# Performance work log

Measured on AMD Instinct MI355X. Metric: run time of the kernel, lower is better.

## Reference

```python
import jax, jax.numpy as jnp
import numpy as np

N = 100000
E = 1600000
F_IN = 128
HID = 64
HEADS = 2
OUT_HEADS = 1
NUM_CLASS = 18
NEG_SLOPE = 0.2


def setup_inputs() -> dict:
    key = jax.random.key(0)
    ks = jax.random.split(key, 12)
    x = jax.random.normal(ks[0], (N, F_IN), dtype=jnp.float32)
    edge_index = jax.random.randint(ks[1], (2, E), 0, N, dtype=jnp.int64)
    s = lambda k, shp, fan: jax.random.normal(k, shp, dtype=jnp.float32) * (1.0 / np.sqrt(fan))
    W0 = s(ks[2], (F_IN, HID), F_IN)
    b0 = jnp.zeros((HID,), dtype=jnp.float32)
    W1 = s(ks[3], (HID, HEADS * HID), HID)
    att_src1 = s(ks[4], (HEADS, HID), HID)
    att_dst1 = s(ks[5], (HEADS, HID), HID)
    b1 = jnp.zeros((HEADS * HID,), dtype=jnp.float32)
    W2 = s(ks[6], (HEADS * HID, OUT_HEADS * NUM_CLASS), HEADS * HID)
    att_src2 = s(ks[7], (OUT_HEADS, NUM_CLASS), NUM_CLASS)
    att_dst2 = s(ks[8], (OUT_HEADS, NUM_CLASS), NUM_CLASS)
    b2 = jnp.zeros((OUT_HEADS * NUM_CLASS,), dtype=jnp.float32)
    return {"x": x, "edge_index": edge_index, "W0": W0, "b0": b0,
            "W1": W1, "att_src1": att_src1, "att_dst1": att_dst1, "b1": b1,
            "W2": W2, "att_src2": att_src2, "att_dst2": att_dst2, "b2": b2}


def gat_conv(x, src, dst, W, att_s, att_d, bias, heads, out_ch):
    n = x.shape[0]
    h = (x @ W).reshape(n, heads, out_ch)              # [N,H,C]
    a_s = jnp.sum(h * att_s, axis=-1)                   # [N,H]
    a_d = jnp.sum(h * att_d, axis=-1)                   # [N,H]
    e = jax.nn.leaky_relu(a_s[src] + a_d[dst], NEG_SLOPE)  # [E,H]
    m = jax.ops.segment_max(e, dst, num_segments=n)
    ex = jnp.exp(e - m[dst])
    denom = jax.ops.segment_sum(ex, dst, num_segments=n)
    alpha = ex / denom[dst]                              # [E,H]
    msg = h[src] * alpha[:, :, None]                     # [E,H,C]
    out = jax.ops.segment_sum(msg, dst, num_segments=n)  # [N,H,C]
    return out.reshape(n, heads * out_ch) + bias


def reference(x, edge_index, W0, b0, W1, att_src1, att_dst1, b1, W2, att_src2, att_dst2, b2):
    n = x.shape[0]
    # PyG GATConv adds self-loops by default
    loops = jnp.arange(n, dtype=edge_index.dtype)
    src = jnp.concatenate([edge_index[0], loops])
    dst = jnp.concatenate([edge_index[1], loops])
    # eval mode: dropout is identity
    h = jax.nn.relu(x @ W0 + b0)
    h = jax.nn.elu(gat_conv(h, src, dst, W1, att_src1, att_dst1, b1, HEADS, HID))
    out = gat_conv(h, src, dst, W2, att_src2, att_dst2, b2, OUT_HEADS, NUM_CLASS)
    return jax.nn.log_softmax(out, axis=-1)
```

## Files before the change

kernel.cpp:

```cpp
#include <hip/hip_runtime.h>
#include <math.h>


#define NEG_SLOPE 0.2f
#define STASH_CAP 128

typedef unsigned short ushort_t;

__device__ __forceinline__ float wmax(float v) {
    for (int o = 32; o; o >>= 1) v = fmaxf(v, __shfl_xor(v, o));
    return v;
}
__device__ __forceinline__ float wsum(float v) {
    for (int o = 32; o; o >>= 1) v += __shfl_xor(v, o);
    return v;
}

__device__ __forceinline__ unsigned bfpack(float a, float b) {
    unsigned ua = __float_as_uint(a);
    unsigned ub = __float_as_uint(b);
    ua = (ua + 0x7fffu + ((ua >> 16) & 1u)) >> 16;
    ub = (ub + 0x7fffu + ((ub >> 16) & 1u)) & 0xffff0000u;
    return ua | ub;
}
__device__ __forceinline__ ushort_t bf16of(float a) {
    unsigned ua = __float_as_uint(a);
    return (ushort_t)((ua + 0x7fffu + ((ua >> 16) & 1u)) >> 16);
}
__device__ __forceinline__ float bflo(unsigned u) { return __uint_as_float(u << 16); }
__device__ __forceinline__ float bfhi(unsigned u) { return __uint_as_float(u & 0xffff0000u); }
__device__ __forceinline__ float bfval(ushort_t u) { return __uint_as_float(((unsigned)u) << 16); }

__global__ void k_deg_init(int* __restrict__ deg, int N) {
    int i = blockIdx.x * blockDim.x + threadIdx.x;
    if (i < N) deg[i] = 1;
}

__global__ __launch_bounds__(256) void k_deg_edges(const int* __restrict__ ei,
                                                   int* __restrict__ deg,
                                                   int E, int cohortBlocks) {
    int c = blockIdx.x & 7;
    int pb = blockIdx.x >> 3;
    int tid = pb * 256 + threadIdx.x;
    int stride = cohortBlocks * 256;
    for (int e = tid; e < E; e += stride) {
        int dst = ei[E + e];
        if (((dst >> 13) & 7) != c) continue;
        atomicAdd(&deg[dst], 1);
    }
}

__global__ __launch_bounds__(256) void k_scan1(const int* __restrict__ deg, int* __restrict__ rs,
                                               int* __restrict__ bsum, int N) {
    __shared__ int s[256];
    int t = threadIdx.x;
    int base = blockIdx.x * 1024;
    int i0 = base + t * 4;
    int d0 = (i0 + 0 < N) ? deg[i0 + 0] : 0;
    int d1 = (i0 + 1 < N) ? deg[i0 + 1] : 0;
    int d2 = (i0 + 2 < N) ? deg[i0 + 2] : 0;
    int d3 = (i0 + 3 < N) ? deg[i0 + 3] : 0;
    int s0 = d0, s1 = s0 + d1, s2 = s1 + d2, s3 = s2 + d3;
    int tsum = s3;
    s[t] = tsum;
    __syncthreads();
    for (int off = 1; off < 256; off <<= 1) {
        int v = (t >= off) ? s[t - off] : 0;
        __syncthreads();
        s[t] += v;
        __syncthreads();
    }
    int excl = s[t] - tsum;
    if (i0 + 0 < N) rs[1 + i0 + 0] = excl + s0;
    if (i0 + 1 < N) rs[1 + i0 + 1] = excl + s1;
    if (i0 + 2 < N) rs[1 + i0 + 2] = excl + s2;
    if (i0 + 3 < N) rs[1 + i0 + 3] = excl + s3;
    if (t == 0) bsum[blockIdx.x] = s[255];
}

__global__ __launch_bounds__(256) void k_scan2(const int* __restrict__ bsum,
                                               int* __restrict__ boff, int NB) {
    __shared__ int s[256];
    int t = threadIdx.x;
    int orig = (t < NB) ? bsum[t] : 0;
    s[t] = orig;
    __syncthreads();
    for (int off = 1; off < 256; off <<= 1) {
        int v = (t >= off) ? s[t - off] : 0;
        __syncthreads();
        s[t] += v;
        __syncthreads();
    }
    if (t < NB) boff[t] = s[t] - orig;
}

__global__ void k_scan3(int* __restrict__ rs, const int* __restrict__ boff,
                        const int* __restrict__ deg, int* __restrict__ cursor, int N) {
    int i = blockIdx.x * blockDim.x + threadIdx.x;
    if (i == 0) rs[0] = 0;
    if (i < N) {
        int v = rs[1 + i] + boff[i >> 10];
        rs[1 + i] = v;
        cursor[i] = v - deg[i] + 1;
    }
}

__global__ __launch_bounds__(256) void k_scatter(const int* __restrict__ ei,
                                                 int* __restrict__ cursor,
                                                 const int* __restrict__ rs,
                                                 int* __restrict__ csr,
                                                 int E, int Etot, int cohortBlocks) {
    int c = blockIdx.x & 7;
    int pb = blockIdx.x >> 3;
    int tid = pb * 256 + threadIdx.x;
    int stride = cohortBlocks * 256;
    for (int e = tid; e < Etot; e += stride) {
        int dst = (e < E) ? ei[E + e] : (e - E);
        if (((dst >> 13) & 7) != c) continue;
        if (e < E) {
            int pos = atomicAdd(&cursor[dst], 1);
            csr[pos] = ei[e];
        } else {
            csr[rs[dst]] = dst;
        }
    }
}

__global__ __launch_bounds__(256) void k_gemm12(const float* __restrict__ x,
                                                const float* __restrict__ W0,
                                                const float* __restrict__ b0,
                                                const float* __restrict__ W1,
                                                const float* __restrict__ as_g,
                                                const float* __restrict__ ad_g,
                                                ushort_t* __restrict__ h1b,
                                                float* __restrict__ as1,
                                                float* __restrict__ ad1, int N) {
    __shared__ float smem[16640];
    float* al  = smem;
    float* wl  = smem + 8448;
    float* al2 = smem;
    int t = threadIdx.x;
    int n0 = blockIdx.x * 64;
    {
        const float4* wg = (const float4*)W0;
        float4* wl4 = (float4*)wl;
#pragma unroll
        for (int i = 0; i < 8; ++i) wl4[t + i * 256] = wg[t + i * 256];
#pragma unroll
        for (int i = 0; i < 8; ++i) {
            int f = t + i * 256;
            int node = f >> 5, q = f & 31;
            int ng = n0 + node; if (ng > N - 1) ng = N - 1;
            float4 v = ((const float4*)x)[(size_t)ng * 32 + q];
            *(float4*)&al[node * 132 + q * 4] = v;
        }
    }
    __syncthreads();
    int colg = t & 15;
    int rowg = t >> 4;
    float4 acc[4];
#pragma unroll
    for (int j = 0; j < 4; ++j) acc[j] = make_float4(0.f, 0.f, 0.f, 0.f);
    for (int k4 = 0; k4 < 128; k4 += 4) {
        float4 w0 = *(float4*)&wl[(k4 + 0) * 64 + colg * 4];
        float4 w1 = *(float4*)&wl[(k4 + 1) * 64 + colg * 4];
        float4 w2 = *(float4*)&wl[(k4 + 2) * 64 + colg * 4];
        float4 w3 = *(float4*)&wl[(k4 + 3) * 64 + colg * 4];
#pragma unroll
        for (int j = 0; j < 4; ++j) {
            float4 a = *(float4*)&al[(rowg * 4 + j) * 132 + k4];
            acc[j].x += a.x * w0.x + a.y * w1.x + a.z * w2.x + a.w * w3.x;
            acc[j].y += a.x * w0.y + a.y * w1.y + a.z * w2.y + a.w * w3.y;
            acc[j].z += a.x * w0.z + a.y * w1.z + a.z * w2.z + a.w * w3.z;
            acc[j].w += a.x * w0.w + a.y * w1.w + a.z * w2.w + a.w * w3.w;
        }
    }
    float4 bb = ((const float4*)b0)[colg];
    float4 h0v[4];
#pragma unroll
    for (int j = 0; j < 4; ++j) {
        h0v[j].x = fmaxf(acc[j].x + bb.x, 0.f);
        h0v[j].y = fmaxf(acc[j].y + bb.y, 0.f);
        h0v[j].z = fmaxf(acc[j].z + bb.z, 0.f);
        h0v[j].w = fmaxf(acc[j].w + bb.w, 0.f);
    }
    __syncthreads();
#pragma unroll
    for (int j = 0; j < 4; ++j)
        *(float4*)&al2[(rowg * 4 + j) * 68 + colg * 4] = h0v[j];
    {
        const float4* wg1 = (const float4*)W1;
        float4* wl4 = (float4*)wl;
#pragma unroll
        for (int i = 0; i < 8; ++i) wl4[t + i * 256] = wg1[t + i * 256];
    }
    __syncthreads();
    int colg2 = t & 31;
    int rowg2 = t >> 5;
    float4 acc2[8];
#pragma unroll
    for (int j = 0; j < 8; ++j) acc2[j] = make_float4(0.f, 0.f, 0.f, 0.f);
    for (int k4 = 0; k4 < 64; k4 += 4) {
        float4 w0 = *(float4*)&wl[(k4 + 0) * 128 + colg2 * 4];
        float4 w1 = *(float4*)&wl[(k4 + 1) * 128 + colg2 * 4];
        float4 w2 = *(float4*)&wl[(k4 + 2) * 128 + colg2 * 4];
        float4 w3 = *(float4*)&wl[(k4 + 3) * 128 + colg2 * 4];
#pragma unroll
        for (int j = 0; j < 8; ++j) {
            float4 a = *(float4*)&al2[(rowg2 * 8 + j) * 68 + k4];
            acc2[j].x += a.x * w0.x + a.y * w1.x + a.z * w2.x + a.w * w3.x;
            acc2[j].y += a.x * w0.y + a.y * w1.y + a.z * w2.y + a.w * w3.y;
            acc2[j].z += a.x * w0.z + a.y * w1.z + a.z * w2.z + a.w * w3.z;
            acc2[j].w += a.x * w0.w + a.y * w1.w + a.z * w2.w + a.w * w3.w;
        }
    }
    float4 asv = ((const float4*)as_g)[colg2];
    float4 adv = ((const float4*)ad_g)[colg2];
    float ps[8], pd[8];
#pragma unroll
    for (int j = 0; j < 8; ++j) {
        ps[j] = acc2[j].x * asv.x + acc2[j].y * asv.y + acc2[j].z * asv.z + acc2[j].w * asv.w;
        pd[j] = acc2[j].x * adv.x + acc2[j].y * adv.y + acc2[j].z * adv.z + acc2[j].w * adv.w;
    }
    for (int o = 1; o < 16; o <<= 1) {
#pragma unroll
        for (int j = 0; j < 8; ++j) {
            ps[j] += __shfl_xor(ps[j], o);
            pd[j] += __shfl_xor(pd[j], o);
        }
    }
#pragma unroll
    for (int j = 0; j < 8; ++j) {
        int n = n0 + rowg2 * 8 + j;
        if (n < N) {
            uint2 pr;
            pr.x = bfpack(acc2[j].x, acc2[j].y);
            pr.y = bfpack(acc2[j].z, acc2[j].w);
            ((uint2*)h1b)[(size_t)n * 32 + colg2] = pr;
        }
    }
    int lane = t & 63;
    if ((lane & 15) == 0) {
        int head = (lane >> 4) & 1;
#pragma unroll
        for (int j = 0; j < 8; ++j) {
            int n = n0 + rowg2 * 8 + j;
            if (n < N) {
                as1[n * 2 + head] = ps[j];
                ad1[n * 2 + head] = pd[j];
            }
        }
    }
}

__global__ __launch_bounds__(256) void k_node_l1(const int* __restrict__ rs,
                                                 const int* __restrict__ csr,
                                                 const ushort_t* __restrict__ h1b,
                                                 const float* __restrict__ as1,
                                                 const float* __restrict__ ad1,
                                                 const float* __restrict__ b1,
                                                 unsigned* __restrict__ aggb, int N) {
    __shared__ float2 stashA[4][128];
    __shared__ float4 stashE[4][STASH_CAP];
    int wid = threadIdx.x >> 6;
    int lane = threadIdx.x & 63;
    int n = (blockIdx.x * 256 + threadIdx.x) >> 6;
    if (n >= N) return;
    int row = rs[n], end = rs[n + 1];
    int deg = end - row;
    float2 adv = ((const float2*)ad1)[n];
    const float2* asp = (const float2*)as1;
    const char* h1base = (const char*)h1b;
    int eg = lane >> 4;
    int fl = lane & 15;
    int head_off = (fl >= 8) ? 64 : 0;
    int flbase = fl * 16;
    float acc[8] = {0.f, 0.f, 0.f, 0.f, 0.f, 0.f, 0.f, 0.f};
    float inv0, inv1;
    if (deg <= 64) {
        bool act = lane < deg;
        int src = act ? csr[row + lane] : 0;
        float2 av = asp[src];
        float e0 = av.x + adv.x, e1 = av.y + adv.y;
        e0 = e0 > 0.f ? e0 : NEG_SLOPE * e0;
        e1 = e1 > 0.f ? e1 : NEG_SLOPE * e1;
        if (!act) { e0 = -INFINITY; e1 = -INFINITY; }
        float m0 = wmax(e0), m1 = wmax(e1);
        float p0 = act ? __expf(e0 - m0) : 0.f;
        float p1 = act ? __expf(e1 - m1) : 0.f;
        inv0 = __builtin_amdgcn_rcpf(wsum(p0));
        inv1 = __builtin_amdgcn_rcpf(wsum(p1));
        stashA[wid][lane] = make_float2(__int_as_float(src), p0);
        stashA[wid][64 + lane] = make_float2(__int_as_float(src), p1);
        int deg8 = (deg + 7) & ~7;
        int b0i = head_off + eg;
        float2 sa0 = stashA[wid][b0i];
        float2 sa1 = stashA[wid][b0i + 4];
        uint4 u0 = *(const uint4*)(h1base + (((unsigned)__float_as_int(sa0.x)) << 8) + flbase);
        uint4 u1 = *(const uint4*)(h1base + (((unsigned)__float_as_int(sa1.x)) << 8) + flbase);
        for (int j = 0; j < deg8; j += 8) {
            int jn = (j + 8 < deg8) ? j + 8 : 0;
            float2 sb0 = stashA[wid][b0i + jn];
            float2 sb1 = stashA[wid][b0i + jn + 4];
            uint4 v0 = *(const uint4*)(h1base + (((unsigned)__float_as_int(sb0.x)) << 8) + flbase);
            uint4 v1 = *(const uint4*)(h1base + (((unsigned)__float_as_int(sb1.x)) << 8) + flbase);
            float a0 = sa0.y, a1 = sa1.y;
            acc[0] += bflo(u0.x) * a0; acc[1] += bfhi(u0.x) * a0;
            acc[2] += bflo(u0.y) * a0; acc[3] += bfhi(u0.y) * a0;
            acc[4] += bflo(u0.z) * a0; acc[5] += bfhi(u0.z) * a0;
            acc[6] += bflo(u0.w) * a0; acc[7] += bfhi(u0.w) * a0;
            acc[0] += bflo(u1.x) * a1; acc[1] += bfhi(u1.x) * a1;
            acc[2] += bflo(u1.y) * a1; acc[3] += bfhi(u1.y) * a1;
            acc[4] += bflo(u1.z) * a1; acc[5] += bfhi(u1.z) * a1;
            acc[6] += bflo(u1.w) * a1; acc[7] += bfhi(u1.w) * a1;
            sa0 = sb0; sa1 = sb1; u0 = v0; u1 = v1;
        }
    } else {
        inv0 = 1.f; inv1 = 1.f;
        float m0 = -INFINITY, m1 = -INFINITY, l0 = 0.f, l1 = 0.f;
        for (int base = row; base < end; base += 64) {
            int idx = base + lane;
            bool act = idx < end;
            int src = act ? csr[idx] : 0;
            float2 av = asp[src];
            float e0 = av.x + adv.x, e1 = av.y + adv.y;
            e0 = e0 > 0.f ? e0 : NEG_SLOPE * e0;
            e1 = e1 > 0.f ? e1 : NEG_SLOPE * e1;
            int sidx = idx - row;
            if (act && sidx < STASH_CAP)
                stashE[wid][sidx] = make_float4(__int_as_float(src), e0, e1, 0.f);
            if (!act) { e0 = -INFINITY; e1 = -INFINITY; }
            float m0n = fmaxf(m0, wmax(e0));
            float m1n = fmaxf(m1, wmax(e1));
            float p0 = act ? __expf(e0 - m0n) : 0.f;
            float p1 = act ? __expf(e1 - m1n) : 0.f;
            l0 = l0 * __expf(m0 - m0n) + wsum(p0);
            l1 = l1 * __expf(m1 - m1n) + wsum(p1);
            m0 = m0n; m1 = m1n;
        }
        float r0 = __builtin_amdgcn_rcpf(l0);
        float r1 = __builtin_amdgcn_rcpf(l1);
        for (int base = row; base < end; base += 64) {
            int idx = base + lane;
            bool act = idx < end;
            int sidx = idx - row;
            int src; float e0, e1;
            if (sidx < STASH_CAP) {
                float4 se = stashE[wid][sidx];
                src = __float_as_int(se.x);
                e0 = se.y; e1 = se.z;
            } else {
                src = act ? csr[idx] : 0;
                float2 av = asp[src];
                e0 = av.x + adv.x; e1 = av.y + adv.y;
                e0 = e0 > 0.f ? e0 : NEG_SLOPE * e0;
                e1 = e1 > 0.f ? e1 : NEG_SLOPE * e1;
            }
            if (!act) src = 0;
            float a0 = act ? __expf(e0 - m0) * r0 : 0.f;
            float a1 = act ? __expf(e1 - m1) * r1 : 0.f;
            stashA[wid][lane] = make_float2(__int_as_float(src), a0);
            stashA[wid][64 + lane] = make_float2(__int_as_float(src), a1);
            int cnt = min(64, end - base);
            for (int j = 0; j < cnt; j += 4) {
                float2 sa = stashA[wid][head_off + j + eg];
                int sj = __float_as_int(sa.x);
                float aj = sa.y;
                uint4 u = *(const uint4*)(h1base + (((unsigned)sj) << 8) + flbase);
                acc[0] += bflo(u.x) * aj; acc[1] += bfhi(u.x) * aj;
                acc[2] += bflo(u.y) * aj; acc[3] += bfhi(u.y) * aj;
                acc[4] += bflo(u.z) * aj; acc[5] += bfhi(u.z) * aj;
                acc[6] += bflo(u.w) * aj; acc[7] += bfhi(u.w) * aj;
            }
        }
    }
#pragma unroll
    for (int i = 0; i < 8; ++i) {
        acc[i] += __shfl_xor(acc[i], 16);
        acc[i] += __shfl_xor(acc[i], 32);
    }
    if (lane < 16) {
        float inv = (lane >= 8) ? inv1 : inv0;
        float4 ba = ((const float4*)b1)[lane * 2];
        float4 bb4 = ((const float4*)b1)[lane * 2 + 1];
        float v[8];
        v[0] = acc[0] * inv + ba.x;  v[1] = acc[1] * inv + ba.y;
        v[2] = acc[2] * inv + ba.z;  v[3] = acc[3] * inv + ba.w;
        v[4] = acc[4] * inv + bb4.x; v[5] = acc[5] * inv + bb4.y;
        v[6] = acc[6] * inv + bb4.z; v[7] = acc[7] * inv + bb4.w;
#pragma unroll
        for (int i = 0; i < 8; ++i) v[i] = v[i] > 0.f ? v[i] : __expf(v[i]) - 1.f;
        uint4 pk;
        pk.x = bfpack(v[0], v[1]); pk.y = bfpack(v[2], v[3]);
        pk.z = bfpack(v[4], v[5]); pk.w = bfpack(v[6], v[7]);
        ((uint4*)aggb)[(size_t)n * 16 + lane] = pk;
    }
}

__global__ __launch_bounds__(256, 4) void k_node2(const unsigned* __restrict__ aggb,
                                                  const float* __restrict__ W2,
                                                  const float* __restrict__ as_g,
                                                  const float* __restrict__ ad_g,
                                                  ushort_t* __restrict__ h2b,
                                                  float* __restrict__ a_s,
                                                  float* __restrict__ a_d, int N) {
    __shared__ float al[64 * 132];
    __shared__ float w2t[20 * 132];
    int t = threadIdx.x;
    int n0 = blockIdx.x * 64;
#pragma unroll
    for (int i = 0; i < 4; ++i) {
        int f = t + i * 256;
        int node = f >> 4, q = f & 15;
        int ng = n0 + node; if (ng > N - 1) ng = N - 1;
        uint4 u = ((const uint4*)aggb)[(size_t)ng * 16 + q];
        float* dst = &al[node * 132 + q * 8];
        dst[0] = bflo(u.x); dst[1] = bfhi(u.x);
        dst[2] = bflo(u.y); dst[3] = bfhi(u.y);
        dst[4] = bflo(u.z); dst[5] = bfhi(u.z);
        dst[6] = bflo(u.w); dst[7] = bfhi(u.w);
    }
    for (int i = t; i < 2560; i += 256) {
        int c = i >> 7, k = i & 127;
        w2t[c * 132 + k] = (c < 18) ? W2[k * 18 + c] : 0.f;
    }
    __syncthreads();
    int node = t >> 2;
    int cq = t & 3;
    int c0 = cq * 5;
    int n = n0 + node;
    float acc[5] = {0.f, 0.f, 0.f, 0.f, 0.f};
#pragma unroll 2
    for (int k4 = 0; k4 < 128; k4 += 4) {
        float4 a = *(float4*)&al[node * 132 + k4];
#pragma unroll
        for (int i = 0; i < 5; ++i) {
            float4 w = *(float4*)&w2t[(c0 + i) * 132 + k4];
            acc[i] += a.x * w.x + a.y * w.y + a.z * w.z + a.w * w.w;
        }
    }
    float ps = 0.f, pd = 0.f;
#pragma unroll
    for (int i = 0; i < 5; ++i) {
        int c = c0 + i;
        float asv = (c < 18) ? as_g[c] : 0.f;
        float adv = (c < 18) ? ad_g[c] : 0.f;
        ps += acc[i] * asv;
        pd += acc[i] * adv;
    }
    ps += __shfl_xor(ps, 1); ps += __shfl_xor(ps, 2);
    pd += __shfl_xor(pd, 1); pd += __shfl_xor(pd, 2);
    if (n < N) {
#pragma unroll
        for (int i = 0; i < 5; ++i) {
            int c = c0 + i;
            if (c < 18) h2b[(size_t)n * 32 + c] = bf16of(acc[i]);
        }
        if (cq == 0) { a_s[n] = ps; a_d[n] = pd; }
    }
}

__global__ __launch_bounds__(256) void k_node_l2(const int* __restrict__ rs,
                                                 const int* __restrict__ csr,
                                                 const ushort_t* __restrict__ h2b,
                                                 const float* __restrict__ as2,
                                                 const float* __restrict__ ad2,
                                                 const float* __restrict__ b2,
                                                 float* __restrict__ out, int N) {
    __shared__ float2 stash[4][STASH_CAP];
    int wid = threadIdx.x >> 6;
    int lane = threadIdx.x & 63;
    int n = (blockIdx.x * 256 + threadIdx.x) >> 6;
    if (n >= N) return;
    int row = rs[n], end = rs[n + 1];
    int deg = end - row;
    float adn = ad2[n];
    int g = lane / 21;
    int c = lane - g * 21;
    int cc = c < 18 ? c : 17;
    float acc = 0.f;
    float post;
    if (deg <= 64) {
        bool act = lane < deg;
        int src = act ? csr[row + lane] : 0;
        float e = as2[src] + adn;
        e = e > 0.f ? e : NEG_SLOPE * e;
        if (!act) e = -INFINITY;
        float m = wmax(e);
        float p = act ? __expf(e - m) : 0.f;
        post = __builtin_amdgcn_rcpf(wsum(p));
        stash[wid][lane] = make_float2(__int_as_float(src), p);
        int o = g;
        for (; o + 3 < deg; o += 6) {
            float2 s0 = stash[wid][o];
            float2 s1 = stash[wid][o + 3];
            int q0 = __float_as_int(s0.x);
            int q1 = __float_as_int(s1.x);
            float v0 = bfval(h2b[(size_t)q0 * 32 + cc]);
            float v1 = bfval(h2b[(size_t)q1 * 32 + cc]);
            acc += s0.y * v0 + s1.y * v1;
        }
        if (o < deg) {
            float2 s0 = stash[wid][o];
            int q0 = __float_as_int(s0.x);
            acc += s0.y * bfval(h2b[(size_t)q0 * 32 + cc]);
        }
    } else {
        post = 1.f;
        float m = -INFINITY, l = 0.f;
        for (int base = row; base < end; base += 64) {
            int idx = base + lane;
            bool act = idx < end;
            int src = act ? csr[idx] : 0;
            float e = as2[src] + adn;
            e = e > 0.f ? e : NEG_SLOPE * e;
            int sidx = idx - row;
            if (act && sidx < STASH_CAP)
                stash[wid][sidx] = make_float2(__int_as_float(src), e);
            if (!act) e = -INFINITY;
            float mn = fmaxf(m, wmax(e));
            float p = act ? __expf(e - mn) : 0.f;
            l = l * __expf(m - mn) + wsum(p);
            m = mn;
        }
        float invl = __builtin_amdgcn_rcpf(l);
        int lim = deg < STASH_CAP ? deg : STASH_CAP;
        for (int o = g; o < lim; o += 3) {
            float2 se = stash[wid][o];
            int src = __float_as_int(se.x);
            float alpha = __expf(se.y - m) * invl;
            acc += alpha * bfval(h2b[(size_t)src * 32 + cc]);
        }
        for (int pos = row + STASH_CAP + g; pos < end; pos += 3) {
            int src = csr[pos];
            float e = as2[src] + adn;
            e = e > 0.f ? e : NEG_SLOPE * e;
            float alpha = __expf(e - m) * invl;
            acc += alpha * bfval(h2b[(size_t)src * 32 + cc]);
        }
    }
    float t1 = __shfl(acc, (lane + 21) & 63);
    float t2 = __shfl(acc, (lane + 42) & 63);
    acc += t1 + t2;
    float bb = (lane < 18) ? b2[lane] : 0.f;
    float v = acc * post + bb;
    float tmx = (lane < 18) ? v : -INFINITY;
    for (int o = 16; o; o >>= 1) tmx = fmaxf(tmx, __shfl_xor(tmx, o));
    float s = (lane < 18) ? __expf(v - tmx) : 0.f;
    for (int o = 16; o; o >>= 1) s += __shfl_xor(s, o);
    float lse = tmx + __logf(s);
    if (lane < 18) out[(size_t)n * 18 + lane] = v - lse;
}

extern "C" void kernel_launch(void* const* d_in, const int* in_sizes, int n_in,
                              void* d_out, int out_size, void* d_ws, size_t ws_size,
                              hipStream_t stream) {
    const float* x      = (const float*)d_in[0];
    const int*   ei     = (const int*)d_in[1];
    const float* W0     = (const float*)d_in[2];
    const float* b0     = (const float*)d_in[3];
    const float* W1     = (const float*)d_in[4];
    const float* att_s1 = (const float*)d_in[5];
    const float* att_d1 = (const float*)d_in[6];
    const float* b1     = (const float*)d_in[7];
    const float* W2     = (const float*)d_in[8];
    const float* att_s2 = (const float*)d_in[9];
    const float* att_d2 = (const float*)d_in[10];
    const float* b2     = (const float*)d_in[11];

    const int N = in_sizes[0] / 128;
    const int E = in_sizes[1] / 2;
    const int Etot = E + N;
    const int NB = (N + 1023) / 1024;
    const int NBLK = (N + 63) / 64;

    char* w = (char*)d_ws;
    ushort_t* h1b  = (ushort_t*)w; w += (size_t)N * 128 * 2;
    unsigned* aggb = (unsigned*)w; w += (size_t)N * 128 * 2;
    float* as1     = (float*)w;    w += (size_t)N * 2 * 4;
    float* ad1     = (float*)w;    w += (size_t)N * 2 * 4;
    ushort_t* h2b  = (ushort_t*)w; w += (size_t)N * 32 * 2;
    float* as2     = (float*)w;    w += (size_t)N * 4;
    float* ad2     = (float*)w;    w += (size_t)N * 4;
    int* deg       = (int*)w;      w += (size_t)N * 4;
    int* rs        = (int*)w;      w += (size_t)(N + 1) * 4;
    int* cursor    = (int*)w;      w += (size_t)N * 4;
    int* bsum      = (int*)w;      w += (size_t)256 * 4;
    int* boff      = (int*)w;      w += (size_t)256 * 4;
    int* csr       = (int*)w;      w += (size_t)Etot * 4;

    float* out = (float*)d_out;

    const int cohortBlocks = 128;

    k_deg_init<<<(N + 255) / 256, 256, 0, stream>>>(deg, N);
    k_deg_edges<<<8 * cohortBlocks, 256, 0, stream>>>(ei, deg, E, cohortBlocks);
    k_scan1<<<NB, 256, 0, stream>>>(deg, rs, bsum, N);
    k_scan2<<<1, 256, 0, stream>>>(bsum, boff, NB);
    k_scan3<<<(N + 255) / 256, 256, 0, stream>>>(rs, boff, deg, cursor, N);
    k_scatter<<<8 * cohortBlocks, 256, 0, stream>>>(ei, cursor, rs, csr, E, Etot, cohortBlocks);

    k_gemm12<<<NBLK, 256, 0, stream>>>(x, W0, b0, W1, att_s1, att_d1, h1b, as1, ad1, N);

    k_node_l1<<<(N * 64 + 255) / 256, 256, 0, stream>>>(rs, csr, h1b, as1, ad1, b1, aggb, N);

    k_node2<<<NBLK, 256, 0, stream>>>(aggb, W2, att_s2, att_d2, h2b, as2, ad2, N);
    k_node_l2<<<(N * 64 + 255) / 256, 256, 0, stream>>>(rs, csr, h2b, as2, ad2, b2, out, N);
}
```

Measured before the change: 462.8 us.

## Record per-edge slot offsets in degree pass and widen gemm blocks to 512 threads

Result: faster. 451.4 us (-2.5%).

```diff
diff --git a/kernel.cpp b/kernel.cpp
--- a/kernel.cpp
+++ b/kernel.cpp
@@ -35,19 +35,10 @@
     int i = blockIdx.x * blockDim.x + threadIdx.x;
     if (i < N) deg[i] = 1;
 }
-
-__global__ __launch_bounds__(256) void k_deg_edges(const int* __restrict__ ei,
-                                                   int* __restrict__ deg,
-                                                   int E, int cohortBlocks) {
-    int c = blockIdx.x & 7;
-    int pb = blockIdx.x >> 3;
-    int tid = pb * 256 + threadIdx.x;
-    int stride = cohortBlocks * 256;
-    for (int e = tid; e < E; e += stride) {
-        int dst = ei[E + e];
-        if (((dst >> 13) & 7) != c) continue;
-        atomicAdd(&deg[dst], 1);
-    }
+__global__ void k_deg_edges(const int* __restrict__ ei, int* __restrict__ deg,
+                            int* __restrict__ eofs, int E) {
+    int e = blockIdx.x * blockDim.x + threadIdx.x;
+    if (e < E) eofs[e] = atomicAdd(&deg[ei[E + e]], 1);
 }
 
 __global__ __launch_bounds__(256) void k_scan1(const int* __restrict__ deg, int* __restrict__ rs,
@@ -94,19 +85,14 @@
     if (t < NB) boff[t] = s[t] - orig;
 }
 
-__global__ void k_scan3(int* __restrict__ rs, const int* __restrict__ boff,
-                        const int* __restrict__ deg, int* __restrict__ cursor, int N) {
+__global__ void k_scan3(int* __restrict__ rs, const int* __restrict__ boff, int N) {
     int i = blockIdx.x * blockDim.x + threadIdx.x;
     if (i == 0) rs[0] = 0;
-    if (i < N) {
-        int v = rs[1 + i] + boff[i >> 10];
-        rs[1 + i] = v;
-        cursor[i] = v - deg[i] + 1;
-    }
+    if (i < N) rs[1 + i] += boff[i >> 10];
 }
 
 __global__ __launch_bounds__(256) void k_scatter(const int* __restrict__ ei,
-                                                 int* __restrict__ cursor,
+                                                 const int* __restrict__ eofs,
                                                  const int* __restrict__ rs,
                                                  int* __restrict__ csr,
                                                  int E, int Etot, int cohortBlocks) {
@@ -117,16 +103,13 @@
     for (int e = tid; e < Etot; e += stride) {
         int dst = (e < E) ? ei[E + e] : (e - E);
         if (((dst >> 13) & 7) != c) continue;
-        if (e < E) {
-            int pos = atomicAdd(&cursor[dst], 1);
-            csr[pos] = ei[e];
-        } else {
-            csr[rs[dst]] = dst;
-        }
-    }
-}
-
-__global__ __launch_bounds__(256) void k_gemm12(const float* __restrict__ x,
+        int src, ofs;
+        if (e < E) { src = ei[e]; ofs = eofs[e]; } else { src = dst; ofs = 0; }
+        csr[rs[dst] + ofs] = src;
+    }
+}
+
+__global__ __launch_bounds__(512) void k_gemm12(const float* __restrict__ x,
                                                 const float* __restrict__ W0,
                                                 const float* __restrict__ b0,
                                                 const float* __restrict__ W1,
@@ -145,10 +128,10 @@
         const float4* wg = (const float4*)W0;
         float4* wl4 = (float4*)wl;
 #pragma unroll
-        for (int i = 0; i < 8; ++i) wl4[t + i * 256] = wg[t + i * 256];
-#pragma unroll
-        for (int i = 0; i < 8; ++i) {
-            int f = t + i * 256;
+        for (int i = 0; i < 4; ++i) wl4[t + i * 512] = wg[t + i * 512];
+#pragma unroll
+        for (int i = 0; i < 4; ++i) {
+            int f = t + i * 512;
             int node = f >> 5, q = f & 31;
             int ng = n0 + node; if (ng > N - 1) ng = N - 1;
             float4 v = ((const float4*)x)[(size_t)ng * 32 + q];
@@ -158,17 +141,17 @@
     __syncthreads();
     int colg = t & 15;
     int rowg = t >> 4;
-    float4 acc[4];
-#pragma unroll
-    for (int j = 0; j < 4; ++j) acc[j] = make_float4(0.f, 0.f, 0.f, 0.f);
+    float4 acc[2];
+#pragma unroll
+    for (int j = 0; j < 2; ++j) acc[j] = make_float4(0.f, 0.f, 0.f, 0.f);
     for (int k4 = 0; k4 < 128; k4 += 4) {
         float4 w0 = *(float4*)&wl[(k4 + 0) * 64 + colg * 4];
         float4 w1 = *(float4*)&wl[(k4 + 1) * 64 + colg * 4];
         float4 w2 = *(float4*)&wl[(k4 + 2) * 64 + colg * 4];
         float4 w3 = *(float4*)&wl[(k4 + 3) * 64 + colg * 4];
 #pragma unroll
-        for (int j = 0; j < 4; ++j) {
-            float4 a = *(float4*)&al[(rowg * 4 + j) * 132 + k4];
+        for (int j = 0; j < 2; ++j) {
+            float4 a = *(float4*)&al[(rowg * 2 + j) * 132 + k4];
             acc[j].x += a.x * w0.x + a.y * w1.x + a.z * w2.x + a.w * w3.x;
             acc[j].y += a.x * w0.y + a.y * w1.y + a.z * w2.y + a.w * w3.y;
             acc[j].z += a.x * w0.z + a.y * w1.z + a.z * w2.z + a.w * w3.z;
@@ -176,9 +159,9 @@
         }
     }
     float4 bb = ((const float4*)b0)[colg];
-    float4 h0v[4];
-#pragma unroll
-    for (int j = 0; j < 4; ++j) {
+    float4 h0v[2];
+#pragma unroll
+    for (int j = 0; j < 2; ++j) {
         h0v[j].x = fmaxf(acc[j].x + bb.x, 0.f);
         h0v[j].y = fmaxf(acc[j].y + bb.y, 0.f);
         h0v[j].z = fmaxf(acc[j].z + bb.z, 0.f);
@@ -186,28 +169,28 @@
     }
     __syncthreads();
 #pragma unroll
-    for (int j = 0; j < 4; ++j)
-        *(float4*)&al2[(rowg * 4 + j) * 68 + colg * 4] = h0v[j];
+    for (int j = 0; j < 2; ++j)
+        *(float4*)&al2[(rowg * 2 + j) * 68 + colg * 4] = h0v[j];
     {
         const float4* wg1 = (const float4*)W1;
         float4* wl4 = (float4*)wl;
 #pragma unroll
-        for (int i = 0; i < 8; ++i) wl4[t + i * 256] = wg1[t + i * 256];
+        for (int i = 0; i < 4; ++i) wl4[t + i * 512] = wg1[t + i * 512];
     }
     __syncthreads();
     int colg2 = t & 31;
     int rowg2 = t >> 5;
-    float4 acc2[8];
-#pragma unroll
-    for (int j = 0; j < 8; ++j) acc2[j] = make_float4(0.f, 0.f, 0.f, 0.f);
+    float4 acc2[4];
+#pragma unroll
+    for (int j = 0; j < 4; ++j) acc2[j] = make_float4(0.f, 0.f, 0.f, 0.f);
     for (int k4 = 0; k4 < 64; k4 += 4) {
         float4 w0 = *(float4*)&wl[(k4 + 0) * 128 + colg2 * 4];
         float4 w1 = *(float4*)&wl[(k4 + 1) * 128 + colg2 * 4];
         float4 w2 = *(float4*)&wl[(k4 + 2) * 128 + colg2 * 4];
         float4 w3 = *(float4*)&wl[(k4 + 3) * 128 + colg2 * 4];
 #pragma unroll
-        for (int j = 0; j < 8; ++j) {
-            float4 a = *(float4*)&al2[(rowg2 * 8 + j) * 68 + k4];
+        for (int j = 0; j < 4; ++j) {
+            float4 a = *(float4*)&al2[(rowg2 * 4 + j) * 68 + k4];
             acc2[j].x += a.x * w0.x + a.y * w1.x + a.z * w2.x + a.w * w3.x;
             acc2[j].y += a.x * w0.y + a.y * w1.y + a.z * w2.y + a.w * w3.y;
             acc2[j].z += a.x * w0.z + a.y * w1.z + a.z * w2.z + a.w * w3.z;
@@ -216,22 +199,22 @@
     }
     float4 asv = ((const float4*)as_g)[colg2];
     float4 adv = ((const float4*)ad_g)[colg2];
-    float ps[8], pd[8];
-#pragma unroll
-    for (int j = 0; j < 8; ++j) {
+    float ps[4], pd[4];
+#pragma unroll
+    for (int j = 0; j < 4; ++j) {
         ps[j] = acc2[j].x * asv.x + acc2[j].y * asv.y + acc2[j].z * asv.z + acc2[j].w * asv.w;
         pd[j] = acc2[j].x * adv.x + acc2[j].y * adv.y + acc2[j].z * adv.z + acc2[j].w * adv.w;
     }
     for (int o = 1; o < 16; o <<= 1) {
 #pragma unroll
-        for (int j = 0; j < 8; ++j) {
+        for (int j = 0; j < 4; ++j) {
             ps[j] += __shfl_xor(ps[j], o);
             pd[j] += __shfl_xor(pd[j], o);
         }
     }
 #pragma unroll
-    for (int j = 0; j < 8; ++j) {
-        int n = n0 + rowg2 * 8 + j;
+    for (int j = 0; j < 4; ++j) {
+        int n = n0 + rowg2 * 4 + j;
         if (n < N) {
             uint2 pr;
             pr.x = bfpack(acc2[j].x, acc2[j].y);
@@ -243,8 +226,8 @@
     if ((lane & 15) == 0) {
         int head = (lane >> 4) & 1;
 #pragma unroll
-        for (int j = 0; j < 8; ++j) {
-            int n = n0 + rowg2 * 8 + j;
+        for (int j = 0; j < 4; ++j) {
+            int n = n0 + rowg2 * 4 + j;
             if (n < N) {
                 as1[n * 2 + head] = ps[j];
                 ad1[n * 2 + head] = pd[j];
@@ -584,23 +567,22 @@
     float* ad2     = (float*)w;    w += (size_t)N * 4;
     int* deg       = (int*)w;      w += (size_t)N * 4;
     int* rs        = (int*)w;      w += (size_t)(N + 1) * 4;
-    int* cursor    = (int*)w;      w += (size_t)N * 4;
     int* bsum      = (int*)w;      w += (size_t)256 * 4;
     int* boff      = (int*)w;      w += (size_t)256 * 4;
+    int* eofs      = (int*)w;      w += (size_t)E * 4;
     int* csr       = (int*)w;      w += (size_t)Etot * 4;
 
     float* out = (float*)d_out;
 
-    const int cohortBlocks = 128;
-
     k_deg_init<<<(N + 255) / 256, 256, 0, stream>>>(deg, N);
-    k_deg_edges<<<8 * cohortBlocks, 256, 0, stream>>>(ei, deg, E, cohortBlocks);
+    k_deg_edges<<<(E + 255) / 256, 256, 0, stream>>>(ei, deg, eofs, E);
     k_scan1<<<NB, 256, 0, stream>>>(deg, rs, bsum, N);
     k_scan2<<<1, 256, 0, stream>>>(bsum, boff, NB);
-    k_scan3<<<(N + 255) / 256, 256, 0, stream>>>(rs, boff, deg, cursor, N);
-    k_scatter<<<8 * cohortBlocks, 256, 0, stream>>>(ei, cursor, rs, csr, E, Etot, cohortBlocks);
-
-    k_gemm12<<<NBLK, 256, 0, stream>>>(x, W0, b0, W1, att_s1, att_d1, h1b, as1, ad1, N);
+    k_scan3<<<(N + 255) / 256, 256, 0, stream>>>(rs, boff, N);
+    const int cohortBlocks = 128;
+    k_scatter<<<8 * cohortBlocks, 256, 0, stream>>>(ei, eofs, rs, csr, E, Etot, cohortBlocks);
+
+    k_gemm12<<<NBLK, 512, 0, stream>>>(x, W0, b0, W1, att_s1, att_d1, h1b, as1, ad1, N);
 
     k_node_l1<<<(N * 64 + 255) / 256, 256, 0, stream>>>(rs, csr, h1b, as1, ad1, b1, aggb, N);
 
```

## Fuse CSR construction into one cooperative kernel with precomputed edge offsets

Applied to the files above, without the earlier changes.

New measurement: 918.3 us. 1.98x slower.

```diff
diff --git a/kernel.cpp b/kernel.cpp
--- a/kernel.cpp
+++ b/kernel.cpp
@@ -1,9 +1,12 @@
 #include <hip/hip_runtime.h>
+#include <hip/hip_cooperative_groups.h>
 #include <math.h>
 
 
 #define NEG_SLOPE 0.2f
 #define STASH_CAP 128
+
+namespace cg = cooperative_groups;
 
 typedef unsigned short ushort_t;
 
@@ -31,97 +34,75 @@
 __device__ __forceinline__ float bfhi(unsigned u) { return __uint_as_float(u & 0xffff0000u); }
 __device__ __forceinline__ float bfval(ushort_t u) { return __uint_as_float(((unsigned)u) << 16); }
 
-__global__ void k_deg_init(int* __restrict__ deg, int N) {
-    int i = blockIdx.x * blockDim.x + threadIdx.x;
-    if (i < N) deg[i] = 1;
-}
-
-__global__ __launch_bounds__(256) void k_deg_edges(const int* __restrict__ ei,
-                                                   int* __restrict__ deg,
-                                                   int E, int cohortBlocks) {
-    int c = blockIdx.x & 7;
-    int pb = blockIdx.x >> 3;
-    int tid = pb * 256 + threadIdx.x;
-    int stride = cohortBlocks * 256;
-    for (int e = tid; e < E; e += stride) {
-        int dst = ei[E + e];
-        if (((dst >> 13) & 7) != c) continue;
-        atomicAdd(&deg[dst], 1);
-    }
-}
-
-__global__ __launch_bounds__(256) void k_scan1(const int* __restrict__ deg, int* __restrict__ rs,
-                                               int* __restrict__ bsum, int N) {
+__global__ __launch_bounds__(256) void k_csr(const int* __restrict__ ei,
+                                             int* __restrict__ deg,
+                                             int* __restrict__ eofs,
+                                             int* __restrict__ rs,
+                                             int* __restrict__ bsum,
+                                             int* __restrict__ boff,
+                                             int* __restrict__ csr,
+                                             int N, int E, int Etot, int NB) {
+    cg::grid_group grid = cg::this_grid();
     __shared__ int s[256];
     int t = threadIdx.x;
-    int base = blockIdx.x * 1024;
-    int i0 = base + t * 4;
-    int d0 = (i0 + 0 < N) ? deg[i0 + 0] : 0;
-    int d1 = (i0 + 1 < N) ? deg[i0 + 1] : 0;
-    int d2 = (i0 + 2 < N) ? deg[i0 + 2] : 0;
-    int d3 = (i0 + 3 < N) ? deg[i0 + 3] : 0;
-    int s0 = d0, s1 = s0 + d1, s2 = s1 + d2, s3 = s2 + d3;
-    int tsum = s3;
-    s[t] = tsum;
-    __syncthreads();
-    for (int off = 1; off < 256; off <<= 1) {
-        int v = (t >= off) ? s[t - off] : 0;
+    int gtid = blockIdx.x * 256 + t;
+    int gstride = gridDim.x * 256;
+    for (int i = gtid; i < N; i += gstride) deg[i] = 1;
+    grid.sync();
+    for (int e = gtid; e < E; e += gstride) eofs[e] = atomicAdd(&deg[ei[E + e]], 1);
+    grid.sync();
+    if ((int)blockIdx.x < NB) {
+        int base = blockIdx.x * 1024;
+        int i0 = base + t * 4;
+        int d0 = (i0 + 0 < N) ? deg[i0 + 0] : 0;
+        int d1 = (i0 + 1 < N) ? deg[i0 + 1] : 0;
+        int d2 = (i0 + 2 < N) ? deg[i0 + 2] : 0;
+        int d3 = (i0 + 3 < N) ? deg[i0 + 3] : 0;
+        int s0 = d0, s1 = s0 + d1, s2 = s1 + d2, s3 = s2 + d3;
+        int tsum = s3;
+        s[t] = tsum;
         __syncthreads();
-        s[t] += v;
+        for (int off = 1; off < 256; off <<= 1) {
+            int v = (t >= off) ? s[t - off] : 0;
+            __syncthreads();
+            s[t] += v;
+            __syncthreads();
+        }
+        int excl = s[t] - tsum;
+        if (i0 + 0 < N) rs[1 + i0 + 0] = excl + s0;
+        if (i0 + 1 < N) rs[1 + i0 + 1] = excl + s1;
+        if (i0 + 2 < N) rs[1 + i0 + 2] = excl + s2;
+        if (i0 + 3 < N) rs[1 + i0 + 3] = excl + s3;
+        if (t == 0) bsum[blockIdx.x] = s[255];
+    }
+    grid.sync();
+    if (blockIdx.x == 0) {
+        int orig = (t < NB) ? bsum[t] : 0;
+        s[t] = orig;
         __syncthreads();
-    }
-    int excl = s[t] - tsum;
-    if (i0 + 0 < N) rs[1 + i0 + 0] = excl + s0;
-    if (i0 + 1 < N) rs[1 + i0 + 1] = excl + s1;
-    if (i0 + 2 < N) rs[1 + i0 + 2] = excl + s2;
-    if (i0 + 3 < N) rs[1 + i0 + 3] = excl + s3;
-    if (t == 0) bsum[blockIdx.x] = s[255];
-}
-
-__global__ __launch_bounds__(256) void k_scan2(const int* __restrict__ bsum,
-                                               int* __restrict__ boff, int NB) {
-    __shared__ int s[256];
-    int t = threadIdx.x;
-    int orig = (t < NB) ? bsum[t] : 0;
-    s[t] = orig;
-    __syncthreads();
-    for (int off = 1; off < 256; off <<= 1) {
-        int v = (t >= off) ? s[t - off] : 0;
-        __syncthreads();
-        s[t] += v;
-        __syncthreads();
-    }
-    if (t < NB) boff[t] = s[t] - orig;
-}
-
-__global__ void k_scan3(int* __restrict__ rs, const int* __restrict__ boff,
-                        const int* __restrict__ deg, int* __restrict__ cursor, int N) {
-    int i = blockIdx.x * blockDim.x + threadIdx.x;
-    if (i == 0) rs[0] = 0;
-    if (i < N) {
-        int v = rs[1 + i] + boff[i >> 10];
-        rs[1 + i] = v;
-        cursor[i] = v - deg[i] + 1;
-    }
-}
-
-__global__ __launch_bounds__(256) void k_scatter(const int* __restrict__ ei,
-                                                 int* __restrict__ cursor,
-                                                 const int* __restrict__ rs,
-                                                 int* __restrict__ csr,
-                                                 int E, int Etot, int cohortBlocks) {
-    int c = blockIdx.x & 7;
-    int pb = blockIdx.x >> 3;
-    int tid = pb * 256 + threadIdx.x;
-    int stride = cohortBlocks * 256;
-    for (int e = tid; e < Etot; e += stride) {
-        int dst = (e < E) ? ei[E + e] : (e - E);
-        if (((dst >> 13) & 7) != c) continue;
-        if (e < E) {
-            int pos = atomicAdd(&cursor[dst], 1);
-            csr[pos] = ei[e];
-        } else {
-            csr[rs[dst]] = dst;
+        for (int off = 1; off < 256; off <<= 1) {
+            int v = (t >= off) ? s[t - off] : 0;
+            __syncthreads();
+            s[t] += v;
+            __syncthreads();
+        }
+        if (t < NB) boff[t] = s[t] - orig;
+    }
+    grid.sync();
+    for (int i = gtid; i < N; i += gstride) rs[1 + i] += boff[i >> 10];
+    if (gtid == 0) rs[0] = 0;
+    grid.sync();
+    {
+        int c = blockIdx.x & 7;
+        int pb = blockIdx.x >> 3;
+        int tid2 = pb * 256 + t;
+        int stride = 128 * 256;
+        for (int e = tid2; e < Etot; e += stride) {
+            int dst = (e < E) ? ei[E + e] : (e - E);
+            if (((dst >> 13) & 7) != c) continue;
+            int src, ofs;
+            if (e < E) { src = ei[e]; ofs = eofs[e]; } else { src = dst; ofs = 0; }
+            csr[rs[dst] + ofs] = src;
         }
     }
 }
@@ -584,21 +565,20 @@
     float* ad2     = (float*)w;    w += (size_t)N * 4;
     int* deg       = (int*)w;      w += (size_t)N * 4;
     int* rs        = (int*)w;      w += (size_t)(N + 1) * 4;
-    int* cursor    = (int*)w;      w += (size_t)N * 4;
     int* bsum      = (int*)w;      w += (size_t)256 * 4;
     int* boff      = (int*)w;      w += (size_t)256 * 4;
+    int* eofs      = (int*)w;      w += (size_t)E * 4;
     int* csr       = (int*)w;      w += (size_t)Etot * 4;
 
     float* out = (float*)d_out;
 
-    const int cohortBlocks = 128;
-
-    k_deg_init<<<(N + 255) / 256, 256, 0, stream>>>(deg, N);
-    k_deg_edges<<<8 * cohortBlocks, 256, 0, stream>>>(ei, deg, E, cohortBlocks);
-    k_scan1<<<NB, 256, 0, stream>>>(deg, rs, bsum, N);
-    k_scan2<<<1, 256, 0, stream>>>(bsum, boff, NB);
-    k_scan3<<<(N + 255) / 256, 256, 0, stream>>>(rs, boff, deg, cursor, N);
-    k_scatter<<<8 * cohortBlocks, 256, 0, stream>>>(ei, cursor, rs, csr, E, Etot, cohortBlocks);
+    {
+        int n_ = N, e_ = E, et_ = Etot, nb_ = NB;
+        void* args[] = {(void*)&ei, (void*)&deg, (void*)&eofs, (void*)&rs,
+                        (void*)&bsum, (void*)&boff, (void*)&csr,
+                        (void*)&n_, (void*)&e_, (void*)&et_, (void*)&nb_};
+        hipLaunchCooperativeKernel((void*)k_csr, dim3(1024), dim3(256), args, 0, stream);
+    }
 
     k_gemm12<<<NBLK, 256, 0, stream>>>(x, W0, b0, W1, att_s1, att_d1, h1b, as1, ad1, N);
 
```

## Record per-edge slot from degree atomics and drop cursor atomics in scatter

Applied to the files above, without the earlier changes.

After: 433.1 us (median of 2 runs). 6.4% less time.

```diff
diff --git a/kernel.cpp b/kernel.cpp
--- a/kernel.cpp
+++ b/kernel.cpp
@@ -35,19 +35,10 @@
     int i = blockIdx.x * blockDim.x + threadIdx.x;
     if (i < N) deg[i] = 1;
 }
-
-__global__ __launch_bounds__(256) void k_deg_edges(const int* __restrict__ ei,
-                                                   int* __restrict__ deg,
-                                                   int E, int cohortBlocks) {
-    int c = blockIdx.x & 7;
-    int pb = blockIdx.x >> 3;
-    int tid = pb * 256 + threadIdx.x;
-    int stride = cohortBlocks * 256;
-    for (int e = tid; e < E; e += stride) {
-        int dst = ei[E + e];
-        if (((dst >> 13) & 7) != c) continue;
-        atomicAdd(&deg[dst], 1);
-    }
+__global__ void k_deg_edges(const int* __restrict__ ei, int* __restrict__ deg,
+                            int* __restrict__ eofs, int E) {
+    int e = blockIdx.x * blockDim.x + threadIdx.x;
+    if (e < E) eofs[e] = atomicAdd(&deg[ei[E + e]], 1);
 }
 
 __global__ __launch_bounds__(256) void k_scan1(const int* __restrict__ deg, int* __restrict__ rs,
@@ -94,19 +85,14 @@
     if (t < NB) boff[t] = s[t] - orig;
 }
 
-__global__ void k_scan3(int* __restrict__ rs, const int* __restrict__ boff,
-                        const int* __restrict__ deg, int* __restrict__ cursor, int N) {
+__global__ void k_scan3(int* __restrict__ rs, const int* __restrict__ boff, int N) {
     int i = blockIdx.x * blockDim.x + threadIdx.x;
     if (i == 0) rs[0] = 0;
-    if (i < N) {
-        int v = rs[1 + i] + boff[i >> 10];
-        rs[1 + i] = v;
-        cursor[i] = v - deg[i] + 1;
-    }
+    if (i < N) rs[1 + i] += boff[i >> 10];
 }
 
 __global__ __launch_bounds__(256) void k_scatter(const int* __restrict__ ei,
-                                                 int* __restrict__ cursor,
+                                                 const int* __restrict__ eofs,
                                                  const int* __restrict__ rs,
                                                  int* __restrict__ csr,
                                                  int E, int Etot, int cohortBlocks) {
@@ -117,12 +103,9 @@
     for (int e = tid; e < Etot; e += stride) {
         int dst = (e < E) ? ei[E + e] : (e - E);
         if (((dst >> 13) & 7) != c) continue;
-        if (e < E) {
-            int pos = atomicAdd(&cursor[dst], 1);
-            csr[pos] = ei[e];
-        } else {
-            csr[rs[dst]] = dst;
-        }
+        int src, ofs;
+        if (e < E) { src = ei[e]; ofs = eofs[e]; } else { src = dst; ofs = 0; }
+        csr[rs[dst] + ofs] = src;
     }
 }
 
@@ -584,21 +567,20 @@
     float* ad2     = (float*)w;    w += (size_t)N * 4;
     int* deg       = (int*)w;      w += (size_t)N * 4;
     int* rs        = (int*)w;      w += (size_t)(N + 1) * 4;
-    int* cursor    = (int*)w;      w += (size_t)N * 4;
     int* bsum      = (int*)w;      w += (size_t)256 * 4;
     int* boff      = (int*)w;      w += (size_t)256 * 4;
+    int* eofs      = (int*)w;      w += (size_t)E * 4;
     int* csr       = (int*)w;      w += (size_t)Etot * 4;
 
     float* out = (float*)d_out;
 
-    const int cohortBlocks = 128;
-
     k_deg_init<<<(N + 255) / 256, 256, 0, stream>>>(deg, N);
-    k_deg_edges<<<8 * cohortBlocks, 256, 0, stream>>>(ei, deg, E, cohortBlocks);
+    k_deg_edges<<<(E + 255) / 256, 256, 0, stream>>>(ei, deg, eofs, E);
     k_scan1<<<NB, 256, 0, stream>>>(deg, rs, bsum, N);
     k_scan2<<<1, 256, 0, stream>>>(bsum, boff, NB);
-    k_scan3<<<(N + 255) / 256, 256, 0, stream>>>(rs, boff, deg, cursor, N);
-    k_scatter<<<8 * cohortBlocks, 256, 0, stream>>>(ei, cursor, rs, csr, E, Etot, cohortBlocks);
+    k_scan3<<<(N + 255) / 256, 256, 0, stream>>>(rs, boff, N);
+    const int cohortBlocks = 128;
+    k_scatter<<<8 * cohortBlocks, 256, 0, stream>>>(ei, eofs, rs, csr, E, Etot, cohortBlocks);
 
     k_gemm12<<<NBLK, 256, 0, stream>>>(x, W0, b0, W1, att_s1, att_d1, h1b, as1, ad1, N);
 
```
